# Kernel tuning notes

Measured on AMD Instinct MI355X. Metric: run time of the kernel, lower is better.

The kernel has to match this reference:

```python
import jax, jax.numpy as jnp
import numpy as np

N = 50000      # nodes
E = 800000     # edges per metapath
M = 3          # metapaths
H = 2          # heads
IN = 128       # in_dim
HID = 64       # hidden
HEAD = HID // H
OUT = 16       # classes
ATT = 128      # atten_dim


def setup_inputs() -> dict:
    key = jax.random.key(0)
    ks = jax.random.split(key, 12)
    s = 0.05
    return {
        "x": jax.random.normal(ks[0], (N, IN), jnp.float32),
        "edge_index": jax.random.randint(ks[1], (M, 2, E), 0, N, dtype=jnp.int64),
        # per-(metapath, head) GCN params
        "W_enc": jax.random.normal(ks[2], (M, H, IN, HID), jnp.float32) * s,
        "b_enc": jnp.zeros((M, H, HID), jnp.float32),
        "W_conv": jax.random.normal(ks[3], (M, H, HID, HID), jnp.float32) * s,
        "b_conv": jnp.zeros((M, H, HID), jnp.float32),
        "W_dec": jax.random.normal(ks[4], (M, H, HID, HEAD), jnp.float32) * s,
        "b_dec": jnp.zeros((M, H, HEAD), jnp.float32),
        # semantic attention params
        "W_s": jax.random.normal(ks[5], (HID, ATT), jnp.float32) * s,
        "b_s": jnp.zeros((ATT,), jnp.float32),
        "q": jax.random.normal(ks[6], (ATT,), jnp.float32) * s,
        # output projection
        "W_o": jax.random.normal(ks[7], (HID, OUT), jnp.float32) * s,
        "b_o": jnp.zeros((OUT,), jnp.float32),
    }


def _lrelu(v, slope=0.1):
    return jnp.where(v > 0, v, slope * v)


def reference(x, edge_index, W_enc, b_enc, W_conv, b_conv, W_dec, b_dec, W_s, b_s, q, W_o, b_o):
    # encoder for all (metapath, head) at once: [M,H,N,HID]
    h = _lrelu(jnp.einsum('ni,mhio->mhno', x, W_enc) + b_enc[:, :, None, :])

    z_list = []
    for m in range(M):  # small fixed number of metapaths
        src = edge_index[m, 0]
        dst = edge_index[m, 1]
        # GCNConv with self-loops + symmetric normalization (PyG semantics)
        deg = jax.ops.segment_sum(jnp.ones(E, jnp.float32), dst, num_segments=N) + 1.0
        inv_sqrt = jax.lax.rsqrt(deg)
        coef = inv_sqrt[src] * inv_sqrt[dst]                 # [E]
        xw = jnp.einsum('hnd,hdo->hno', h[m], W_conv[m])     # [H,N,HID]
        msg = xw[:, src, :] * coef[None, :, None]            # [H,E,HID] gather
        agg = jax.vmap(lambda mm: jax.ops.segment_sum(mm, dst, num_segments=N))(msg)
        agg = agg + xw * (1.0 / deg)[None, :, None]          # self-loop term (norm = 1/deg)
        agg = agg + b_conv[m][:, None, :]
        hh = _lrelu(agg)
        dec = jnp.einsum('hnd,hdo->hno', hh, W_dec[m]) + b_dec[m][:, None, :]  # [H,N,HEAD]
        z_list.append(jnp.transpose(dec, (1, 0, 2)).reshape(N, HID))           # head concat

    zs = jnp.stack(z_list)                                   # [M,N,HID]
    # semantic attention over metapaths
    hs = jnp.tanh(jnp.einsum('mnd,da->mna', zs, W_s) + b_s)
    beta = jax.nn.softmax(jnp.einsum('mna,a->mn', hs, q).mean(axis=1))  # [M]
    Z = jnp.einsum('m,mnd->nd', beta, zs)                    # [N,HID]
    out = jax.nn.log_softmax(Z @ W_o + b_o, axis=-1)         # [N,OUT]
    return out, beta
```

## Files before the change

kernel.cpp:

```cpp
#include <hip/hip_runtime.h>

#define NN 50000
#define EE 800000
#define MM 3
#define HH 2
#define IND 128
#define HIDD 64
#define HEADD 32
#define OUTD 16
#define ATTD 128

#define NBKT 64
#define BSZ 782

#define NG4 200000
#define BBLK 196
#define QCAP 13200

#define GLS 136
#define XWN 50048
#define PN  50048

typedef unsigned char u8;
typedef unsigned short u16;
typedef unsigned long long u64;
typedef short bf16x8 __attribute__((ext_vector_type(8)));
typedef unsigned short u16x8 __attribute__((ext_vector_type(8)));
typedef u64 u64x2 __attribute__((ext_vector_type(2)));
typedef unsigned int u32x4 __attribute__((ext_vector_type(4)));
typedef float f32x2 __attribute__((ext_vector_type(2)));
typedef float f32x4 __attribute__((ext_vector_type(4)));

__device__ __forceinline__ float lrelu(float v) { return v > 0.f ? v : 0.1f * v; }

__device__ __forceinline__ float fast_tanh(float x) {
    float ax = fabsf(x);
    float e = __expf(-2.0f * ax);
    float t = (1.0f - e) * __builtin_amdgcn_rcpf(1.0f + e);
    return copysignf(t, x);
}

__device__ __forceinline__ u16 f2b(float f) {
    union { float f; unsigned int u; } v; v.f = f;
    unsigned int r = v.u + 0x7fffu + ((v.u >> 16) & 1u);
    return (u16)(r >> 16);
}
__device__ __forceinline__ float b2f(u16 u) {
    union { unsigned int u; float f; } v; v.u = ((unsigned int)u) << 16; return v.f;
}

__device__ __forceinline__ u8 f2e4hw(float f) {
    int r = __builtin_amdgcn_cvt_pk_fp8_f32(f, f, 0, false);
    return (u8)(r & 0xff);
}

__device__ __forceinline__ void acc16(f32x2* acc, u32x4 w) {
#pragma unroll
    for (int i = 0; i < 4; i++) {
        acc[2 * i]     += __builtin_amdgcn_cvt_pk_f32_fp8(w[i], false);
        acc[2 * i + 1] += __builtin_amdgcn_cvt_pk_f32_fp8(w[i], true);
    }
}

__global__ __launch_bounds__(256) void k_bucket(const int* __restrict__ ei,
                                                u64* __restrict__ queues,
                                                int* __restrict__ gcur) {
    __shared__ int cnt[NBKT];
    __shared__ int base[NBKT];
    const int m = blockIdx.y, tid = threadIdx.x;
    const int4* s4 = (const int4*)(ei + (size_t)m * 2 * EE);
    const int4* d4 = (const int4*)(ei + (size_t)m * 2 * EE + EE);
    const int q0 = blockIdx.x * 1024;
    if (tid < NBKT) cnt[tid] = 0;
    __syncthreads();
#pragma unroll
    for (int i = 0; i < 4; i++) {
        int q = q0 + i * 256 + tid;
        if (q < NG4) {
            int4 v = d4[q];
            atomicAdd(&cnt[v.x / BSZ], 1);
            atomicAdd(&cnt[v.y / BSZ], 1);
            atomicAdd(&cnt[v.z / BSZ], 1);
            atomicAdd(&cnt[v.w / BSZ], 1);
        }
    }
    __syncthreads();
    if (tid < NBKT) { base[tid] = atomicAdd(&gcur[m * NBKT + tid], cnt[tid]); cnt[tid] = 0; }
    __syncthreads();
#pragma unroll
    for (int i = 0; i < 4; i++) {
        int q = q0 + i * 256 + tid;
        if (q < NG4) {
            int4 dv = d4[q];
            int4 sv = s4[q];
            int ds[4] = {dv.x, dv.y, dv.z, dv.w};
            int ss[4] = {sv.x, sv.y, sv.z, sv.w};
#pragma unroll
            for (int e = 0; e < 4; e++) {
                int b = ds[e] / BSZ;
                int slot = base[b] + atomicAdd(&cnt[b], 1);
                if (slot < QCAP) {
                    u64 pk = ((u64)(unsigned)ds[e] << 32) | (unsigned)ss[e];
                    queues[((size_t)(m * NBKT + b)) * QCAP + slot] = pk;
                }
            }
        }
    }
}

__global__ void k_pscan(const int* __restrict__ gcur, int* __restrict__ pbase) {
    int t = threadIdx.x;
    if (t < MM) {
        int run = 0;
        for (int b = 0; b < NBKT; b++) {
            int L = gcur[t * NBKT + b]; if (L > QCAP) L = QCAP;
            pbase[t * NBKT + b] = run; run += L;
        }
    }
}

__global__ __launch_bounds__(512) void k_csr(const u64* __restrict__ queues,
                                             const int* __restrict__ gcur,
                                             const int* __restrict__ pbase,
                                             int* __restrict__ ofs,
                                             float* __restrict__ rs,
                                             int* __restrict__ sorted) {
    __shared__ int cnt[BSZ];
    __shared__ int wscan[8];
    const int m = blockIdx.y;
    const int b = blockIdx.x;
    const int tid = threadIdx.x;
    const int lane = tid & 63, w = tid >> 6;
    int qlen = gcur[m * NBKT + b]; if (qlen > QCAP) qlen = QCAP;
    const u64* q = queues + ((size_t)(m * NBKT + b)) * QCAP;
    const u64x2* q2 = (const u64x2*)q;
    const int dlo = b * BSZ;
    const int nd = min(dlo + BSZ, NN) - dlo;
    const int n2 = qlen >> 1;
    for (int i = tid; i < BSZ; i += 512) cnt[i] = 0;
    __syncthreads();
    for (int i = tid; i < n2; i += 512) {
        u64x2 e = q2[i];
        atomicAdd(&cnt[(int)(e.x >> 32) - dlo], 1);
        atomicAdd(&cnt[(int)(e.y >> 32) - dlo], 1);
    }
    if (tid == 0 && (qlen & 1))
        atomicAdd(&cnt[(int)(q[qlen - 1] >> 32) - dlo], 1);
    __syncthreads();
    const int c0 = tid * 2;
    int v0 = (c0 < BSZ) ? cnt[c0] : 0;
    int v1 = (c0 + 1 < BSZ) ? cnt[c0 + 1] : 0;
    int s = v0 + v1;
    int vv = s;
    for (int off = 1; off < 64; off <<= 1) { int t = __shfl_up(vv, off); if (lane >= off) vv += t; }
    if (lane == 63) wscan[w] = vv;
    __syncthreads();
    if (tid == 0) { int run = 0; for (int j = 0; j < 8; j++) { int t = wscan[j]; wscan[j] = run; run += t; } }
    __syncthreads();
    int excl = wscan[w] + vv - s;
    int g0 = pbase[m * NBKT + b] + excl;
    int g1 = g0 + v0;
    if (c0 < nd) {
        ofs[(size_t)m * (NN + 1) + dlo + c0] = g0;
        rs[(size_t)m * NN + dlo + c0] = rsqrtf((float)(v0 + 1));
    }
    if (c0 + 1 < nd) {
        ofs[(size_t)m * (NN + 1) + dlo + c0 + 1] = g1;
        rs[(size_t)m * NN + dlo + c0 + 1] = rsqrtf((float)(v1 + 1));
    }
    if (b == NBKT - 1 && tid == 0)
        ofs[(size_t)m * (NN + 1) + NN] = EE;
    __syncthreads();
    if (c0 < BSZ) cnt[c0] = g0;
    if (c0 + 1 < BSZ) cnt[c0 + 1] = g1;
    __syncthreads();
    int* srt = sorted + (size_t)m * EE;
    for (int i = tid; i < n2; i += 512) {
        u64x2 e = q2[i];
        int p0 = atomicAdd(&cnt[(int)(e.x >> 32) - dlo], 1);
        srt[p0] = (int)(e.x & 0xffffffffu);
        int p1 = atomicAdd(&cnt[(int)(e.y >> 32) - dlo], 1);
        srt[p1] = (int)(e.y & 0xffffffffu);
    }
    if (tid == 0 && (qlen & 1)) {
        u64 e = q[qlen - 1];
        int p0 = atomicAdd(&cnt[(int)(e >> 32) - dlo], 1);
        srt[p0] = (int)(e & 0xffffffffu);
    }
}

__global__ __launch_bounds__(256) void k_dhist(const int* __restrict__ ofs_all,
                                               int* __restrict__ bins,
                                               int* __restrict__ bbase) {
    __shared__ int lh[64];
    const int m = blockIdx.y, blk = blockIdx.x, tid = threadIdx.x;
    if (tid < 64) lh[tid] = 0;
    __syncthreads();
    int n = blk * 256 + tid;
    if (n < NN) {
        const int* ofs = ofs_all + (size_t)m * (NN + 1);
        int d = ofs[n + 1] - ofs[n];
        atomicAdd(&lh[d > 63 ? 63 : d], 1);
    }
    __syncthreads();
    if (tid < 64)
        bbase[((size_t)m * BBLK + blk) * 64 + tid] = atomicAdd(&bins[m * 64 + tid], lh[tid]);
}

__global__ void k_dscan(int* __restrict__ bins) {
    int m = threadIdx.x;
    if (m < MM) {
        int run = 0;
        for (int b = 63; b >= 0; b--) {
            int cb = bins[m * 64 + b];
            bins[m * 64 + b] = run;
            run += cb;
        }
    }
}

__global__ __launch_bounds__(256) void k_dscat(const int* __restrict__ ofs_all,
                                               const int* __restrict__ bins,
                                               const int* __restrict__ bbase,
                                               int* __restrict__ perm_all) {
    __shared__ int lh[64];
    const int m = blockIdx.y, blk = blockIdx.x, tid = threadIdx.x;
    if (tid < 64) lh[tid] = 0;
    __syncthreads();
    int n = blk * 256 + tid;
    int* perm = perm_all + (size_t)m * PN;
    if (n < NN) {
        const int* ofs = ofs_all + (size_t)m * (NN + 1);
        int d = ofs[n + 1] - ofs[n];
        int b = d > 63 ? 63 : d;
        int lr = atomicAdd(&lh[b], 1);
        int slot = bins[m * 64 + b] + bbase[((size_t)m * BBLK + blk) * 64 + b] + lr;
        perm[slot] = n;
    } else if (n < PN) {
        perm[n] = NN;
    }
}

__global__ __launch_bounds__(256) void k_prep(const float* __restrict__ We, const float* __restrict__ Wc,
                                              const float* __restrict__ Wd, const float* __restrict__ Ws,
                                              u16* __restrict__ wbe, u16* __restrict__ wbc,
                                              u16* __restrict__ wbd, u16* __restrict__ wbs) {
    int t = blockIdx.x * 256 + threadIdx.x;
    if (t >= 11776) return;
    bf16x8 val;
    u16* dst;
    if (t < 6144) {
        int m = t >> 11, r = t & 2047;
        int nt = r >> 8, ks = (r >> 6) & 3, lane = r & 63;
        int n = nt * 16 + (lane & 15), h = n >> 6, o = n & 63;
        int kb = ks * 32 + (lane >> 4) * 8;
        const float* w = We + ((size_t)(m * 2 + h) * 128) * 64;
#pragma unroll
        for (int j = 0; j < 8; j++) val[j] = (short)f2b(w[(size_t)(kb + j) * 64 + o]);
        dst = wbe + ((size_t)m * 2048 + r) * 8;
    } else if (t < 9216) {
        int u = t - 6144;
        int m = u >> 10, r = u & 1023;
        int nt = r >> 7, ks = (r >> 6) & 1, lane = r & 63;
        int h = nt >> 2, o = (nt & 3) * 16 + (lane & 15);
        int kb = ks * 32 + (lane >> 4) * 8;
        const float* w = Wc + ((size_t)(m * 2 + h) * 64) * 64;
#pragma unroll
        for (int j = 0; j < 8; j++) val[j] = (short)f2b(w[(size_t)(kb + j) * 64 + o]);
        dst = wbc + ((size_t)m * 1024 + r) * 8;
    } else if (t < 10752) {
        int u = t - 9216;
        int m = u >> 9, r = u & 511;
        int nt = r >> 7, ks = (r >> 6) & 1, lane = r & 63;
        int h = nt >> 1, o = (nt & 1) * 16 + (lane & 15);
        int kb = ks * 32 + (lane >> 4) * 8;
        const float* w = Wd + ((size_t)(m * 2 + h) * 64) * 32;
#pragma unroll
        for (int j = 0; j < 8; j++) val[j] = (short)f2b(w[(size_t)(kb + j) * 32 + o]);
        dst = wbd + ((size_t)m * 512 + r) * 8;
    } else {
        int r = t - 10752;
        int nt = r >> 7, ks = (r >> 6) & 1, lane = r & 63;
        int n = nt * 16 + (lane & 15);
        int kb = ks * 32 + (lane >> 4) * 8;
#pragma unroll
        for (int j = 0; j < 8; j++) val[j] = (short)f2b(Ws[(size_t)(kb + j) * 128 + n]);
        dst = wbs + (size_t)r * 8;
    }
    *(bf16x8*)dst = val;
}

#define HLS 133
__global__ __launch_bounds__(256) void k_encconv(const float* __restrict__ x,
                                                 const u16* __restrict__ wbe_all,
                                                 const float* __restrict__ be_all,
                                                 const u16* __restrict__ wbc_all,
                                                 const float* __restrict__ rs_all,
                                                 u8* __restrict__ xw_all) {
    __shared__ float hl[64 * HLS];
    const int m = blockIdx.y;
    const int tid = threadIdx.x, lane = tid & 63, wave = tid >> 6;
    const int quad = lane >> 4, c16 = lane & 15;
    const int row = blockIdx.x * 64 + wave * 16 + c16;
    const bool ok = row < NN;
    const bf16x8* wbE = (const bf16x8*)(wbe_all + (size_t)m * 2048 * 8);
    const float* be = be_all + m * 2 * 64;
    const float* rs = rs_all + (size_t)m * NN;
    u8* xw = xw_all + (size_t)m * XWN * 128;
    f32x4 zero = {0.f, 0.f, 0.f, 0.f};
    f32x4 acc[8];
#pragma unroll
    for (int nt = 0; nt < 8; nt++) acc[nt] = zero;
#pragma unroll
    for (int ks = 0; ks < 4; ks++) {
        bf16x8 a = {0, 0, 0, 0, 0, 0, 0, 0};
        if (ok) {
            const float* xp = x + (size_t)row * 128 + ks * 32 + quad * 8;
            float4 xa = *(const float4*)xp;
            float4 xb = *(const float4*)(xp + 4);
            a[0] = (short)f2b(xa.x); a[1] = (short)f2b(xa.y);
            a[2] = (short)f2b(xa.z); a[3] = (short)f2b(xa.w);
            a[4] = (short)f2b(xb.x); a[5] = (short)f2b(xb.y);
            a[6] = (short)f2b(xb.z); a[7] = (short)f2b(xb.w);
        }
#pragma unroll
        for (int nt = 0; nt < 8; nt++)
            acc[nt] = __builtin_amdgcn_mfma_f32_16x16x32_bf16(a, wbE[(nt * 4 + ks) * 64 + lane], acc[nt], 0, 0, 0);
    }
    const int rbl = wave * 16 + quad * 4;
#pragma unroll
    for (int nt = 0; nt < 8; nt++) {
        int col = nt * 16 + c16, hh = col >> 6, o = col & 63;
        float bias = be[hh * 64 + o];
#pragma unroll
        for (int j = 0; j < 4; j++) {
            int rl = rbl + j;
            int rg = blockIdx.x * 64 + rl;
            hl[rl * HLS + col] = (rg < NN) ? lrelu(acc[nt][j] + bias) : 0.f;
        }
    }
    __syncthreads();
    const bf16x8* wbC = (const bf16x8*)(wbc_all + (size_t)m * 1024 * 8);
    f32x4 cacc[8];
#pragma unroll
    for (int nt = 0; nt < 8; nt++) cacc[nt] = zero;
    const int rl = wave * 16 + c16;
#pragma unroll
    for (int ks = 0; ks < 2; ks++) {
        bf16x8 a0, a1;
        const float* hp = &hl[rl * HLS + ks * 32 + quad * 8];
#pragma unroll
        for (int j = 0; j < 8; j++) { a0[j] = (short)f2b(hp[j]); a1[j] = (short)f2b(hp[64 + j]); }
#pragma unroll
        for (int nt = 0; nt < 8; nt++)
            cacc[nt] = __builtin_amdgcn_mfma_f32_16x16x32_bf16(nt < 4 ? a0 : a1, wbC[(nt * 2 + ks) * 64 + lane], cacc[nt], 0, 0, 0);
    }
    float rsv[4];
#pragma unroll
    for (int j = 0; j < 4; j++) {
        int r = blockIdx.x * 64 + rbl + j;
        rsv[j] = (r < NN) ? rs[r] * 64.f : 0.f;
    }
#pragma unroll
    for (int nt = 0; nt < 8; nt++) {
        int col = nt * 16 + c16;
#pragma unroll
        for (int j = 0; j < 4; j++) {
            int r = blockIdx.x * 64 + rbl + j;
            xw[(size_t)r * 128 + col] = f2e4hw(cacc[nt][j] * rsv[j]);
        }
    }
}

__global__ __launch_bounds__(512) void k_gpost(const int* __restrict__ sorted_all,
                                               const int* __restrict__ ofs_all,
                                               const int* __restrict__ perm_all,
                                               const float* __restrict__ rs_all,
                                               const u8* __restrict__ xw_all,
                                               const float* __restrict__ bconv_all,
                                               const u16* __restrict__ wbd_all,
                                               const float* __restrict__ bdec_all,
                                               const u16* __restrict__ wbs,
                                               const float* __restrict__ bs,
                                               const float* __restrict__ qv,
                                               u16* __restrict__ z_all,
                                               float* __restrict__ score) {
    __shared__ u16 shm[64 * GLS];
    __shared__ float spart[8];
    __shared__ int pml[64];
    u16* ggl = shm;
    float* zl = (float*)shm;
    const int m = blockIdx.y;
    const int tid = threadIdx.x, lane = tid & 63, wave = tid >> 6;
    const int* sorted = sorted_all + (size_t)m * EE;
    const int* ofs = ofs_all + (size_t)m * (NN + 1);
    const int* perm = perm_all + (size_t)m * PN;
    const float* rs = rs_all + (size_t)m * NN;
    const u8* xw = xw_all + (size_t)m * XWN * 128;
    const float* bconv = bconv_all + m * 2 * 64;
    const float* bdec = bdec_all + m * 2 * 32;
    u16* z = z_all + (size_t)m * NN * 64;

    if (tid < 64) pml[tid] = perm[blockIdx.x * 64 + tid];

    {
        const int g = lane >> 3, c = lane & 7;
        const int dst = perm[blockIdx.x * 64 + wave * 8 + g];
        const bool on = dst < NN;
        int beg = 0, deg = 0;
        if (on) { beg = ofs[dst]; deg = ofs[dst + 1] - beg; }
        int degmax = max(deg, __shfl_xor(deg, 8));
        degmax = max(degmax, __shfl_xor(degmax, 16));
        degmax = max(degmax, __shfl_xor(degmax, 32));
        const int coff = c * 16;

        auto lidx = [&](int j) -> int {
            int t = j + (c & 3);
            return (t < deg) ? sorted[beg + t] : NN;
        };
        auto lrow = [&](int iv, u32x4* wv) {
#pragma unroll
            for (int k = 0; k < 4; k++) {
                int s = __shfl(iv, (lane & 0x38) + k);
                wv[k] = *(const u32x4*)&xw[(size_t)(unsigned)s * 128 + coff];
            }
        };

        f32x2 acc[8];
#pragma unroll
        for (int i = 0; i < 8; i++) acc[i] = 0.f;

        int i0 = lidx(0);
        int i1 = lidx(4);
        {
            int sd = on ? dst : NN;
            u32x4 w = *(const u32x4*)&xw[(size_t)sd * 128 + coff];
            acc16(acc, w);
        }
        u32x4 wA[4], wB[4];
        lrow(i0, wA);
        const int nch = ((degmax + 7) >> 3) * 2;
        for (int ch = 0; ch < nch; ch += 2) {
            lrow(i1, wB);
            i0 = lidx(ch * 4 + 8);
#pragma unroll
            for (int k = 0; k < 4; k++) acc16(acc, wA[k]);
            lrow(i0, wA);
            i1 = lidx(ch * 4 + 12);
#pragma unroll
            for (int k = 0; k < 4; k++) acc16(acc, wB[k]);
        }

        float rsv = on ? rs[dst] * (1.f / 64.f) : 0.f;
        u16x8 o0, o1;
#pragma unroll
        for (int i = 0; i < 4; i++) {
            o0[2 * i]     = f2b(acc[i].x * rsv);
            o0[2 * i + 1] = f2b(acc[i].y * rsv);
            o1[2 * i]     = f2b(acc[i + 4].x * rsv);
            o1[2 * i + 1] = f2b(acc[i + 4].y * rsv);
        }
        u16* gp = &ggl[(wave * 8 + g) * GLS + coff];
        *(u16x8*)gp = o0;
        *(u16x8*)(gp + 8) = o1;
    }
    __syncthreads();

    f32x4 zero = {0.f, 0.f, 0.f, 0.f};
    const int quad = lane >> 4, c16 = lane & 15;
    const int wq = wave & 3, hi = wave >> 2;
    const int rl = wq * 16 + c16;
    const bf16x8* wd = (const bf16x8*)(wbd_all + (size_t)m * 512 * 8);
    f32x4 pacc[2];
    pacc[0] = zero; pacc[1] = zero;
#pragma unroll
    for (int ks = 0; ks < 2; ks++) {
        bf16x8 a;
        int k0 = ks * 32 + quad * 8;
        u16x8 gv = *(const u16x8*)&ggl[rl * GLS + hi * 64 + k0];
#pragma unroll
        for (int j = 0; j < 8; j++)
            a[j] = (short)f2b(lrelu(b2f(gv[j]) + bconv[hi * 64 + k0 + j]));
#pragma unroll
        for (int nt2 = 0; nt2 < 2; nt2++) {
            int nt = hi * 2 + nt2;
            pacc[nt2] = __builtin_amdgcn_mfma_f32_16x16x32_bf16(a, wd[(nt * 2 + ks) * 64 + lane], pacc[nt2], 0, 0, 0);
        }
    }
    __syncthreads();
    {
        const int rbl = wq * 16 + quad * 4;
#pragma unroll
        for (int nt2 = 0; nt2 < 2; nt2++) {
            int nt = hi * 2 + nt2;
            int col = nt * 16 + c16, hh = col >> 5, o = col & 31;
            float bias = bdec[hh * 32 + o];
#pragma unroll
            for (int j = 0; j < 4; j++) {
                int rl2 = rbl + j;
                zl[rl2 * 68 + col] = (pml[rl2] < NN) ? (pacc[nt2][j] + bias) : 0.f;
            }
        }
    }
    __syncthreads();

    {
        int rl2 = tid >> 3, cq = tid & 7;
        int node = pml[rl2];
        if (node < NN) {
#pragma unroll
            for (int i = 0; i < 2; i++) {
                int c4 = (cq * 2 + i) * 4;
                float4 zv = *(const float4*)&zl[rl2 * 68 + c4];
                ushort4 o;
                o.x = f2b(zv.x); o.y = f2b(zv.y); o.z = f2b(zv.z); o.w = f2b(zv.w);
                *(ushort4*)&z[(size_t)node * 64 + c4] = o;
            }
        }
    }
    float s = 0.f;
    {
        const bf16x8* wsb = (const bf16x8*)wbs;
        f32x4 sa[4];
#pragma unroll
        for (int nt2 = 0; nt2 < 4; nt2++) sa[nt2] = zero;
#pragma unroll
        for (int ks = 0; ks < 2; ks++) {
            bf16x8 a;
            const float* zp = &zl[rl * 68 + ks * 32 + quad * 8];
            f32x4 z0 = *(const f32x4*)zp;
            f32x4 z1 = *(const f32x4*)(zp + 4);
            a[0] = (short)f2b(z0[0]); a[1] = (short)f2b(z0[1]);
            a[2] = (short)f2b(z0[2]); a[3] = (short)f2b(z0[3]);
            a[4] = (short)f2b(z1[0]); a[5] = (short)f2b(z1[1]);
            a[6] = (short)f2b(z1[2]); a[7] = (short)f2b(z1[3]);
#pragma unroll
            for (int nt2 = 0; nt2 < 4; nt2++) {
                int nt = hi * 4 + nt2;
                sa[nt2] = __builtin_amdgcn_mfma_f32_16x16x32_bf16(a, wsb[(nt * 2 + ks) * 64 + lane], sa[nt2], 0, 0, 0);
            }
        }
        const int rbl = wq * 16 + quad * 4;
#pragma unroll
        for (int nt2 = 0; nt2 < 4; nt2++) {
            int nt = hi * 4 + nt2;
            int col = nt * 16 + c16;
            float qc = qv[col], bb = bs[col];
#pragma unroll
            for (int j = 0; j < 4; j++) {
                if (pml[rbl + j] < NN) s += fast_tanh(sa[nt2][j] + bb) * qc;
            }
        }
#pragma unroll
        for (int off = 1; off < 64; off <<= 1) s += __shfl_xor(s, off);
    }
    if (lane == 0) spart[wave] = s;
    __syncthreads();
    if (tid == 0) {
        float t = spart[0] + spart[1] + spart[2] + spart[3]
                + spart[4] + spart[5] + spart[6] + spart[7];
        atomicAdd(&score[m], t);
    }
}

__global__ void k_beta(const float* __restrict__ score, float* __restrict__ beta_ws,
                       float* __restrict__ out) {
    if (threadIdx.x == 0) {
        float s0 = score[0] / (float)NN, s1 = score[1] / (float)NN, s2 = score[2] / (float)NN;
        float mx = fmaxf(s0, fmaxf(s1, s2));
        float e0 = expf(s0 - mx), e1 = expf(s1 - mx), e2 = expf(s2 - mx);
        float inv = 1.f / (e0 + e1 + e2);
        beta_ws[0] = e0 * inv; beta_ws[1] = e1 * inv; beta_ws[2] = e2 * inv;
        out[800000] = e0 * inv; out[800001] = e1 * inv; out[800002] = e2 * inv;
    }
}

__global__ __launch_bounds__(256) void k_out(const u16* __restrict__ z,
                                             const float* __restrict__ beta,
                                             const float* __restrict__ Wo,
                                             const float* __restrict__ bo,
                                             float* __restrict__ out) {
    __shared__ float Zt[64 * 68];
    __shared__ float Wl[64 * 16];
    __shared__ float bl[16];
    const int tid = threadIdx.x, nbase = blockIdx.x * 64;
    float b0 = beta[0], b1 = beta[1], b2 = beta[2];
    for (int qq = tid; qq < 64 * 16; qq += 256) {
        int node = qq >> 4, k4 = qq & 15;
        int ng = nbase + node;
        float4 v = make_float4(0.f, 0.f, 0.f, 0.f);
        if (ng < NN) {
            ushort4 z0 = *(const ushort4*)&z[((size_t)0 * NN + ng) * 64 + k4 * 4];
            ushort4 z1 = *(const ushort4*)&z[((size_t)1 * NN + ng) * 64 + k4 * 4];
            ushort4 z2 = *(const ushort4*)&z[((size_t)2 * NN + ng) * 64 + k4 * 4];
            v.x = b0 * b2f(z0.x) + b1 * b2f(z1.x) + b2 * b2f(z2.x);
            v.y = b0 * b2f(z0.y) + b1 * b2f(z1.y) + b2 * b2f(z2.y);
            v.z = b0 * b2f(z0.z) + b1 * b2f(z1.z) + b2 * b2f(z2.z);
            v.w = b0 * b2f(z0.w) + b1 * b2f(z1.w) + b2 * b2f(z2.w);
        }
        *(float4*)&Zt[node * 68 + k4 * 4] = v;
    }
    for (int qq = tid; qq < 64 * 16 / 4; qq += 256)
        ((float4*)Wl)[qq] = ((const float4*)Wo)[qq];
    if (tid < 16) bl[tid] = bo[tid];
    __syncthreads();

    const int node = tid >> 2, cg = tid & 3;
    float4 a = make_float4(bl[cg * 4 + 0], bl[cg * 4 + 1], bl[cg * 4 + 2], bl[cg * 4 + 3]);
    for (int k = 0; k < 64; k++) {
        float zv = Zt[node * 68 + k];
        float4 w = *(const float4*)&Wl[k * 16 + cg * 4];
        a.x = fmaf(zv, w.x, a.x);
        a.y = fmaf(zv, w.y, a.y);
        a.z = fmaf(zv, w.z, a.z);
        a.w = fmaf(zv, w.w, a.w);
    }
    float mx = fmaxf(fmaxf(a.x, a.y), fmaxf(a.z, a.w));
    mx = fmaxf(mx, __shfl_xor(mx, 1));
    mx = fmaxf(mx, __shfl_xor(mx, 2));
    float sm = expf(a.x - mx) + expf(a.y - mx) + expf(a.z - mx) + expf(a.w - mx);
    sm += __shfl_xor(sm, 1);
    sm += __shfl_xor(sm, 2);
    float lse = mx + logf(sm);
    int ng = nbase + node;
    if (ng < NN) {
        float4 r = make_float4(a.x - lse, a.y - lse, a.z - lse, a.w - lse);
        *(float4*)&out[(size_t)ng * 16 + cg * 4] = r;
    }
}

extern "C" void kernel_launch(void* const* d_in, const int* in_sizes, int n_in,
                              void* d_out, int out_size, void* d_ws, size_t ws_size,
                              hipStream_t stream) {
    const float* x      = (const float*)d_in[0];
    const int*   ei     = (const int*)d_in[1];
    const float* W_enc  = (const float*)d_in[2];
    const float* b_enc  = (const float*)d_in[3];
    const float* W_conv = (const float*)d_in[4];
    const float* b_conv = (const float*)d_in[5];
    const float* W_dec  = (const float*)d_in[6];
    const float* b_dec  = (const float*)d_in[7];
    const float* W_s    = (const float*)d_in[8];
    const float* b_s    = (const float*)d_in[9];
    const float* qv     = (const float*)d_in[10];
    const float* W_o    = (const float*)d_in[11];
    const float* b_o    = (const float*)d_in[12];
    float* out = (float*)d_out;

    char* ws = (char*)d_ws;
    size_t off = 0;
    auto alloc = [&](size_t bytes) -> char* {
        char* p = ws + off;
        off = (off + bytes + 255) & ~(size_t)255;
        return p;
    };
    int*   row_ofs = (int*)alloc((size_t)MM * (NN + 1) * 4);
    float* rs      = (float*)alloc((size_t)MM * NN * 4);
    int*   sorted  = (int*)alloc((size_t)MM * EE * 4);
    u64*   queues  = (u64*)alloc((size_t)MM * NBKT * QCAP * 8);
    int*   gcur    = (int*)alloc((size_t)MM * NBKT * 4);
    int*   pbase   = (int*)alloc((size_t)MM * NBKT * 4);
    float* score   = (float*)alloc(64);
    float* beta_ws = (float*)alloc(64);
    u16*   wbe     = (u16*)alloc((size_t)MM * 2048 * 8 * 2);
    u16*   wbc     = (u16*)alloc((size_t)MM * 1024 * 8 * 2);
    u16*   wbd     = (u16*)alloc((size_t)MM * 512 * 8 * 2);
    u16*   wbs     = (u16*)alloc((size_t)1024 * 8 * 2);
    u8*    xw_buf  = (u8*)alloc((size_t)MM * XWN * 128);
    u16*   z_buf   = (u16*)alloc((size_t)MM * NN * 64 * 2);
    int*   perm    = (int*)alloc((size_t)MM * PN * 4);
    int*   bins    = (int*)alloc((size_t)MM * 64 * 4);
    int*   bbase   = (int*)alloc((size_t)MM * BBLK * 64 * 4);

    hipMemsetAsync(gcur, 0, (size_t)MM * NBKT * 4, stream);
    hipMemsetAsync(score, 0, 16, stream);
    hipMemsetAsync(bins, 0, (size_t)MM * 64 * 4, stream);

    dim3 gbkt(BBLK, MM);
    dim3 gcsr(NBKT, MM);
    k_bucket<<<gbkt, 256, 0, stream>>>(ei, queues, gcur);
    k_pscan<<<1, 64, 0, stream>>>(gcur, pbase);
    k_csr<<<gcsr, 512, 0, stream>>>(queues, gcur, pbase, row_ofs, rs, sorted);
    k_prep<<<46, 256, 0, stream>>>(W_enc, W_conv, W_dec, W_s, wbe, wbc, wbd, wbs);

    dim3 gdeg(BBLK, MM);
    k_dhist<<<gdeg, 256, 0, stream>>>(row_ofs, bins, bbase);
    k_dscan<<<1, 64, 0, stream>>>(bins);
    k_dscat<<<gdeg, 256, 0, stream>>>(row_ofs, bins, bbase, perm);

    const int GB = (NN + 63) / 64;
    dim3 gmm(GB, MM);
    k_encconv<<<gmm, 256, 0, stream>>>(x, wbe, b_enc, wbc, rs, xw_buf);
    k_gpost<<<gmm, 512, 0, stream>>>(sorted, row_ofs, perm, rs, xw_buf,
                                     b_conv, wbd, b_dec, wbs, b_s, qv,
                                     z_buf, score);
    k_beta<<<1, 64, 0, stream>>>(score, beta_ws, out);
    k_out<<<GB, 256, 0, stream>>>(z_buf, beta_ws, W_o, b_o, out);
}
```

Baseline: 262.8 us.

## Build CSR with global degree atomics and direct scatter instead of bucket queues

Replaces the two-pass bucketed queue CSR build (bucket into 64 coarse queues, then per-bucket local sort) with a global-atomic degree count, a block-sum plus scan for row offsets, and a direct scatter of sources using per-node cursor atomics. The degree histogram used for the degree-sorted permutation is folded into the offsets kernel, so the separate histogram and scan kernels go away. This avoids writing and re-reading the 8-byte packed queue entries, but puts global atomics on random node addresses and scatters sorted writes uncoalesced. It also adds two extra memsets of node-sized arrays.

```diff
diff --git a/kernel.cpp b/kernel.cpp
--- a/kernel.cpp
+++ b/kernel.cpp
@@ -15,7 +15,6 @@
 
 #define NG4 200000
 #define BBLK 196
-#define QCAP 13200
 
 #define GLS 136
 #define XWN 50048
@@ -26,7 +25,6 @@
 typedef unsigned long long u64;
 typedef short bf16x8 __attribute__((ext_vector_type(8)));
 typedef unsigned short u16x8 __attribute__((ext_vector_type(8)));
-typedef u64 u64x2 __attribute__((ext_vector_type(2)));
 typedef unsigned int u32x4 __attribute__((ext_vector_type(4)));
 typedef float f32x2 __attribute__((ext_vector_type(2)));
 typedef float f32x4 __attribute__((ext_vector_type(4)));
@@ -62,31 +60,104 @@
     }
 }
 
-__global__ __launch_bounds__(256) void k_bucket(const int* __restrict__ ei,
-                                                u64* __restrict__ queues,
-                                                int* __restrict__ gcur) {
-    __shared__ int cnt[NBKT];
-    __shared__ int base[NBKT];
+__global__ __launch_bounds__(256) void k_deg(const int* __restrict__ ei,
+                                             int* __restrict__ deg) {
     const int m = blockIdx.y, tid = threadIdx.x;
-    const int4* s4 = (const int4*)(ei + (size_t)m * 2 * EE);
     const int4* d4 = (const int4*)(ei + (size_t)m * 2 * EE + EE);
+    int* dg = deg + (size_t)m * NN;
     const int q0 = blockIdx.x * 1024;
-    if (tid < NBKT) cnt[tid] = 0;
-    __syncthreads();
 #pragma unroll
     for (int i = 0; i < 4; i++) {
         int q = q0 + i * 256 + tid;
         if (q < NG4) {
             int4 v = d4[q];
-            atomicAdd(&cnt[v.x / BSZ], 1);
-            atomicAdd(&cnt[v.y / BSZ], 1);
-            atomicAdd(&cnt[v.z / BSZ], 1);
-            atomicAdd(&cnt[v.w / BSZ], 1);
-        }
-    }
-    __syncthreads();
-    if (tid < NBKT) { base[tid] = atomicAdd(&gcur[m * NBKT + tid], cnt[tid]); cnt[tid] = 0; }
-    __syncthreads();
+            atomicAdd(&dg[v.x], 1);
+            atomicAdd(&dg[v.y], 1);
+            atomicAdd(&dg[v.z], 1);
+            atomicAdd(&dg[v.w], 1);
+        }
+    }
+}
+
+__global__ __launch_bounds__(512) void k_bsum(const int* __restrict__ deg,
+                                              int* __restrict__ bsum) {
+    __shared__ int ws[8];
+    const int m = blockIdx.y, b = blockIdx.x, tid = threadIdx.x;
+    const int lo = b * BSZ;
+    const int n = min(lo + BSZ, NN) - lo;
+    int s = 0;
+    for (int i = tid; i < n; i += 512) s += deg[(size_t)m * NN + lo + i];
+#pragma unroll
+    for (int off = 32; off; off >>= 1) s += __shfl_down(s, off);
+    if ((tid & 63) == 0) ws[tid >> 6] = s;
+    __syncthreads();
+    if (tid == 0) {
+        int t = 0;
+#pragma unroll
+        for (int j = 0; j < 8; j++) t += ws[j];
+        bsum[m * 64 + b] = t;
+    }
+}
+
+__global__ __launch_bounds__(512) void k_ofs(const int* __restrict__ deg,
+                                             const int* __restrict__ bsum,
+                                             int* __restrict__ ofs,
+                                             float* __restrict__ rs,
+                                             int* __restrict__ bins,
+                                             int* __restrict__ bbase) {
+    __shared__ int wscan[8];
+    __shared__ int lh[64];
+    __shared__ int sbase;
+    const int m = blockIdx.y, b = blockIdx.x, tid = threadIdx.x;
+    const int lane = tid & 63, w = tid >> 6;
+    const int lo = b * BSZ;
+    const int n = min(lo + BSZ, NN) - lo;
+    if (tid < 64) lh[tid] = 0;
+    if (tid == 0) {
+        int r = 0;
+        for (int j = 0; j < b; j++) r += bsum[m * 64 + j];
+        sbase = r;
+    }
+    __syncthreads();
+    const int c0 = tid * 2;
+    int v0 = (c0 < n) ? deg[(size_t)m * NN + lo + c0] : 0;
+    int v1 = (c0 + 1 < n) ? deg[(size_t)m * NN + lo + c0 + 1] : 0;
+    int s = v0 + v1;
+    int vv = s;
+    for (int off = 1; off < 64; off <<= 1) { int t = __shfl_up(vv, off); if (lane >= off) vv += t; }
+    if (lane == 63) wscan[w] = vv;
+    __syncthreads();
+    if (tid == 0) { int run = 0; for (int j = 0; j < 8; j++) { int t = wscan[j]; wscan[j] = run; run += t; } }
+    __syncthreads();
+    int excl = wscan[w] + vv - s;
+    int g0 = sbase + excl;
+    if (c0 < n) {
+        ofs[(size_t)m * (NN + 1) + lo + c0] = g0;
+        rs[(size_t)m * NN + lo + c0] = rsqrtf((float)(v0 + 1));
+        atomicAdd(&lh[v0 > 63 ? 63 : v0], 1);
+    }
+    if (c0 + 1 < n) {
+        ofs[(size_t)m * (NN + 1) + lo + c0 + 1] = g0 + v0;
+        rs[(size_t)m * NN + lo + c0 + 1] = rsqrtf((float)(v1 + 1));
+        atomicAdd(&lh[v1 > 63 ? 63 : v1], 1);
+    }
+    if (b == NBKT - 1 && tid == 0) ofs[(size_t)m * (NN + 1) + NN] = EE;
+    __syncthreads();
+    if (tid < 64)
+        bbase[((size_t)m * NBKT + b) * 64 + tid] = atomicAdd(&bins[m * 64 + tid], lh[tid]);
+}
+
+__global__ __launch_bounds__(256) void k_scat(const int* __restrict__ ei,
+                                              const int* __restrict__ ofs,
+                                              int* __restrict__ cur,
+                                              int* __restrict__ sorted) {
+    const int m = blockIdx.y, tid = threadIdx.x;
+    const int4* s4 = (const int4*)(ei + (size_t)m * 2 * EE);
+    const int4* d4 = (const int4*)(ei + (size_t)m * 2 * EE + EE);
+    const int* of = ofs + (size_t)m * (NN + 1);
+    int* cu = cur + (size_t)m * NN;
+    int* srt = sorted + (size_t)m * EE;
+    const int q0 = blockIdx.x * 1024;
 #pragma unroll
     for (int i = 0; i < 4; i++) {
         int q = q0 + i * 256 + tid;
@@ -97,148 +168,44 @@
             int ss[4] = {sv.x, sv.y, sv.z, sv.w};
 #pragma unroll
             for (int e = 0; e < 4; e++) {
-                int b = ds[e] / BSZ;
-                int slot = base[b] + atomicAdd(&cnt[b], 1);
-                if (slot < QCAP) {
-                    u64 pk = ((u64)(unsigned)ds[e] << 32) | (unsigned)ss[e];
-                    queues[((size_t)(m * NBKT + b)) * QCAP + slot] = pk;
-                }
+                int slot = of[ds[e]] + atomicAdd(&cu[ds[e]], 1);
+                srt[slot] = ss[e];
             }
         }
     }
 }
 
-__global__ void k_pscan(const int* __restrict__ gcur, int* __restrict__ pbase) {
-    int t = threadIdx.x;
-    if (t < MM) {
-        int run = 0;
-        for (int b = 0; b < NBKT; b++) {
-            int L = gcur[t * NBKT + b]; if (L > QCAP) L = QCAP;
-            pbase[t * NBKT + b] = run; run += L;
-        }
-    }
-}
-
-__global__ __launch_bounds__(512) void k_csr(const u64* __restrict__ queues,
-                                             const int* __restrict__ gcur,
-                                             const int* __restrict__ pbase,
-                                             int* __restrict__ ofs,
-                                             float* __restrict__ rs,
-                                             int* __restrict__ sorted) {
-    __shared__ int cnt[BSZ];
-    __shared__ int wscan[8];
-    const int m = blockIdx.y;
-    const int b = blockIdx.x;
-    const int tid = threadIdx.x;
-    const int lane = tid & 63, w = tid >> 6;
-    int qlen = gcur[m * NBKT + b]; if (qlen > QCAP) qlen = QCAP;
-    const u64* q = queues + ((size_t)(m * NBKT + b)) * QCAP;
-    const u64x2* q2 = (const u64x2*)q;
-    const int dlo = b * BSZ;
-    const int nd = min(dlo + BSZ, NN) - dlo;
-    const int n2 = qlen >> 1;
-    for (int i = tid; i < BSZ; i += 512) cnt[i] = 0;
-    __syncthreads();
-    for (int i = tid; i < n2; i += 512) {
-        u64x2 e = q2[i];
-        atomicAdd(&cnt[(int)(e.x >> 32) - dlo], 1);
-        atomicAdd(&cnt[(int)(e.y >> 32) - dlo], 1);
-    }
-    if (tid == 0 && (qlen & 1))
-        atomicAdd(&cnt[(int)(q[qlen - 1] >> 32) - dlo], 1);
-    __syncthreads();
-    const int c0 = tid * 2;
-    int v0 = (c0 < BSZ) ? cnt[c0] : 0;
-    int v1 = (c0 + 1 < BSZ) ? cnt[c0 + 1] : 0;
-    int s = v0 + v1;
-    int vv = s;
-    for (int off = 1; off < 64; off <<= 1) { int t = __shfl_up(vv, off); if (lane >= off) vv += t; }
-    if (lane == 63) wscan[w] = vv;
-    __syncthreads();
-    if (tid == 0) { int run = 0; for (int j = 0; j < 8; j++) { int t = wscan[j]; wscan[j] = run; run += t; } }
-    __syncthreads();
-    int excl = wscan[w] + vv - s;
-    int g0 = pbase[m * NBKT + b] + excl;
-    int g1 = g0 + v0;
-    if (c0 < nd) {
-        ofs[(size_t)m * (NN + 1) + dlo + c0] = g0;
-        rs[(size_t)m * NN + dlo + c0] = rsqrtf((float)(v0 + 1));
-    }
-    if (c0 + 1 < nd) {
-        ofs[(size_t)m * (NN + 1) + dlo + c0 + 1] = g1;
-        rs[(size_t)m * NN + dlo + c0 + 1] = rsqrtf((float)(v1 + 1));
-    }
-    if (b == NBKT - 1 && tid == 0)
-        ofs[(size_t)m * (NN + 1) + NN] = EE;
-    __syncthreads();
-    if (c0 < BSZ) cnt[c0] = g0;
-    if (c0 + 1 < BSZ) cnt[c0 + 1] = g1;
-    __syncthreads();
-    int* srt = sorted + (size_t)m * EE;
-    for (int i = tid; i < n2; i += 512) {
-        u64x2 e = q2[i];
-        int p0 = atomicAdd(&cnt[(int)(e.x >> 32) - dlo], 1);
-        srt[p0] = (int)(e.x & 0xffffffffu);
-        int p1 = atomicAdd(&cnt[(int)(e.y >> 32) - dlo], 1);
-        srt[p1] = (int)(e.y & 0xffffffffu);
-    }
-    if (tid == 0 && (qlen & 1)) {
-        u64 e = q[qlen - 1];
-        int p0 = atomicAdd(&cnt[(int)(e >> 32) - dlo], 1);
-        srt[p0] = (int)(e & 0xffffffffu);
-    }
-}
-
-__global__ __launch_bounds__(256) void k_dhist(const int* __restrict__ ofs_all,
-                                               int* __restrict__ bins,
-                                               int* __restrict__ bbase) {
-    __shared__ int lh[64];
-    const int m = blockIdx.y, blk = blockIdx.x, tid = threadIdx.x;
-    if (tid < 64) lh[tid] = 0;
-    __syncthreads();
-    int n = blk * 256 + tid;
-    if (n < NN) {
-        const int* ofs = ofs_all + (size_t)m * (NN + 1);
-        int d = ofs[n + 1] - ofs[n];
-        atomicAdd(&lh[d > 63 ? 63 : d], 1);
-    }
-    __syncthreads();
-    if (tid < 64)
-        bbase[((size_t)m * BBLK + blk) * 64 + tid] = atomicAdd(&bins[m * 64 + tid], lh[tid]);
-}
-
-__global__ void k_dscan(int* __restrict__ bins) {
-    int m = threadIdx.x;
-    if (m < MM) {
-        int run = 0;
-        for (int b = 63; b >= 0; b--) {
-            int cb = bins[m * 64 + b];
-            bins[m * 64 + b] = run;
-            run += cb;
-        }
-    }
-}
-
-__global__ __launch_bounds__(256) void k_dscat(const int* __restrict__ ofs_all,
+__global__ __launch_bounds__(512) void k_dscat(const int* __restrict__ deg,
                                                const int* __restrict__ bins,
                                                const int* __restrict__ bbase,
                                                int* __restrict__ perm_all) {
+    __shared__ int st[64];
     __shared__ int lh[64];
-    const int m = blockIdx.y, blk = blockIdx.x, tid = threadIdx.x;
+    const int m = blockIdx.y, b = blockIdx.x, tid = threadIdx.x;
+    const int lo = b * BSZ;
+    const int n = min(lo + BSZ, NN) - lo;
+    int* perm = perm_all + (size_t)m * PN;
     if (tid < 64) lh[tid] = 0;
-    __syncthreads();
-    int n = blk * 256 + tid;
-    int* perm = perm_all + (size_t)m * PN;
-    if (n < NN) {
-        const int* ofs = ofs_all + (size_t)m * (NN + 1);
-        int d = ofs[n + 1] - ofs[n];
-        int b = d > 63 ? 63 : d;
-        int lr = atomicAdd(&lh[b], 1);
-        int slot = bins[m * 64 + b] + bbase[((size_t)m * BBLK + blk) * 64 + b] + lr;
-        perm[slot] = n;
-    } else if (n < PN) {
-        perm[n] = NN;
-    }
+    if (tid == 0) {
+        int run = 0;
+        for (int j = 63; j >= 0; j--) { st[j] = run; run += bins[m * 64 + j]; }
+    }
+    __syncthreads();
+    const int c0 = tid * 2;
+    if (c0 < n) {
+        int d = deg[(size_t)m * NN + lo + c0];
+        int bin = d > 63 ? 63 : d;
+        int lr = atomicAdd(&lh[bin], 1);
+        perm[st[bin] + bbase[((size_t)m * NBKT + b) * 64 + bin] + lr] = lo + c0;
+    }
+    if (c0 + 1 < n) {
+        int d = deg[(size_t)m * NN + lo + c0 + 1];
+        int bin = d > 63 ? 63 : d;
+        int lr = atomicAdd(&lh[bin], 1);
+        perm[st[bin] + bbase[((size_t)m * NBKT + b) * 64 + bin] + lr] = lo + c0 + 1;
+    }
+    if (b == NBKT - 1 && tid < PN - NN)
+        perm[NN + tid] = NN;
 }
 
 __global__ __launch_bounds__(256) void k_prep(const float* __restrict__ We, const float* __restrict__ Wc,
@@ -657,9 +624,9 @@
     int*   row_ofs = (int*)alloc((size_t)MM * (NN + 1) * 4);
     float* rs      = (float*)alloc((size_t)MM * NN * 4);
     int*   sorted  = (int*)alloc((size_t)MM * EE * 4);
-    u64*   queues  = (u64*)alloc((size_t)MM * NBKT * QCAP * 8);
-    int*   gcur    = (int*)alloc((size_t)MM * NBKT * 4);
-    int*   pbase   = (int*)alloc((size_t)MM * NBKT * 4);
+    int*   deg     = (int*)alloc((size_t)MM * NN * 4);
+    int*   cur     = (int*)alloc((size_t)MM * NN * 4);
+    int*   bsum    = (int*)alloc((size_t)MM * 64 * 4);
     float* score   = (float*)alloc(64);
     float* beta_ws = (float*)alloc(64);
     u16*   wbe     = (u16*)alloc((size_t)MM * 2048 * 8 * 2);
@@ -670,23 +637,21 @@
     u16*   z_buf   = (u16*)alloc((size_t)MM * NN * 64 * 2);
     int*   perm    = (int*)alloc((size_t)MM * PN * 4);
     int*   bins    = (int*)alloc((size_t)MM * 64 * 4);
-    int*   bbase   = (int*)alloc((size_t)MM * BBLK * 64 * 4);
-
-    hipMemsetAsync(gcur, 0, (size_t)MM * NBKT * 4, stream);
+    int*   bbase   = (int*)alloc((size_t)MM * NBKT * 64 * 4);
+
+    hipMemsetAsync(deg, 0, (size_t)MM * NN * 4, stream);
+    hipMemsetAsync(cur, 0, (size_t)MM * NN * 4, stream);
+    hipMemsetAsync(bins, 0, (size_t)MM * 64 * 4, stream);
     hipMemsetAsync(score, 0, 16, stream);
-    hipMemsetAsync(bins, 0, (size_t)MM * 64 * 4, stream);
-
-    dim3 gbkt(BBLK, MM);
-    dim3 gcsr(NBKT, MM);
-    k_bucket<<<gbkt, 256, 0, stream>>>(ei, queues, gcur);
-    k_pscan<<<1, 64, 0, stream>>>(gcur, pbase);
-    k_csr<<<gcsr, 512, 0, stream>>>(queues, gcur, pbase, row_ofs, rs, sorted);
+
+    dim3 gedge(BBLK, MM);
+    dim3 gbkt(NBKT, MM);
+    k_deg<<<gedge, 256, 0, stream>>>(ei, deg);
+    k_bsum<<<gbkt, 512, 0, stream>>>(deg, bsum);
+    k_ofs<<<gbkt, 512, 0, stream>>>(deg, bsum, row_ofs, rs, bins, bbase);
+    k_scat<<<gedge, 256, 0, stream>>>(ei, row_ofs, cur, sorted);
+    k_dscat<<<gbkt, 512, 0, stream>>>(deg, bins, bbase, perm);
     k_prep<<<46, 256, 0, stream>>>(W_enc, W_conv, W_dec, W_s, wbe, wbc, wbd, wbs);
-
-    dim3 gdeg(BBLK, MM);
-    k_dhist<<<gdeg, 256, 0, stream>>>(row_ofs, bins, bbase);
-    k_dscan<<<1, 64, 0, stream>>>(bins);
-    k_dscat<<<gdeg, 256, 0, stream>>>(row_ofs, bins, bbase, perm);
 
     const int GB = (NN + 63) / 64;
     dim3 gmm(GB, MM);
```

Measured after the change: 445.5 us. 1.7x slower.
